# Kernel optimization log

Hardware: AMD Instinct MI355X
Metric: run time of the kernel (lower is better)

Reference implementation:

```python
import jax, jax.numpy as jnp
import numpy as np

B, T, S, H = 4, 256, 1024, 256


def setup_inputs() -> dict:
    key = jax.random.key(0)
    k1, k2, k3, k4, k5, k6 = jax.random.split(key, 6)
    query = jax.random.normal(k1, (B, T, H), dtype=jnp.float32)
    encoder_outputs = jax.random.normal(k2, (B, S, H), dtype=jnp.float32)
    src_lengths = jax.random.randint(k3, (B,), 1, S + 1).astype(jnp.int64)
    scale = 1.0 / np.sqrt(H)
    W_h = jax.random.normal(k4, (H, H), dtype=jnp.float32) * scale
    W_s = jax.random.normal(k5, (H, H), dtype=jnp.float32) * scale
    v = jax.random.normal(k6, (H,), dtype=jnp.float32) * scale
    return {
        "query": query,
        "encoder_outputs": encoder_outputs,
        "src_lengths": src_lengths,
        "W_h": W_h,
        "W_s": W_s,
        "v": v,
    }


def reference(query, encoder_outputs, src_lengths, W_h, W_s, v):
    # score(h_i, s_j) = v^T tanh(W_h h_i + W_s s_j)
    # project once per sequence, then broadcast-add over (tgt, src)
    q_proj = jnp.einsum("bth,hk->btk", query, W_h)            # (B, T, H)
    e_proj = jnp.einsum("bsh,hk->bsk", encoder_outputs, W_s)  # (B, S, H)
    # (B, T, S, H) additive intermediate -> reduce with v
    feats = jnp.tanh(q_proj[:, :, None, :] + e_proj[:, None, :, :])
    scores = jnp.einsum("btsh,h->bts", feats, v)              # (B, T, S)
    # mask padding positions (src positions >= src_lengths[b])
    valid = jnp.arange(scores.shape[-1])[None, :] < src_lengths[:, None]  # (B, S)
    scores = jnp.where(valid[:, None, :], scores, jnp.finfo(scores.dtype).min)
    attn = jax.nn.softmax(scores, axis=-1)                    # (B, T, S)
    attn_out = jnp.einsum("bts,bsh->bth", attn, encoder_outputs)  # (B, T, H)
    return attn_out
```

## Files before the change

### kernel.cpp

```cpp
#include <hip/hip_runtime.h>
#include <math.h>

#define NB 4
#define NT 256
#define NS 1024
#define NH 256
#define TT 4
#define SBK 256
#define NSQ (NS / SBK)
#define BS (NB * NS)

static constexpr float CTWO   = 2.8853900817779268f;
static constexpr float LOG2E  = 1.4426950408889634f;
static constexpr float ACLAMP = 62.0f;

__global__ __launch_bounds__(256) void proj_kernel(const float* __restrict__ Q,
                                                   const float* __restrict__ E,
                                                   const float* __restrict__ W_h,
                                                   const float* __restrict__ W_s,
                                                   float* __restrict__ tq,
                                                   float* __restrict__ te4) {
  __shared__ float As[32][68];
  __shared__ float Bs[32][68];
  const int tid = threadIdx.x;
  int r0 = blockIdx.x * 64;
  const int n0 = blockIdx.y * 64;
  const bool is_q = (r0 < NB * NT);
  const float* A;
  const float* W;
  if (is_q) { A = Q; W = W_h; }
  else      { A = E; W = W_s; r0 -= NB * NT; }
  const int tx = tid & 15;
  const int ty = tid >> 4;
  float acc[4][4] = {};
  for (int k0 = 0; k0 < NH; k0 += 32) {
    {
      const int r = tid >> 2;
      const int kq = (tid & 3) * 8;
      const float* src = A + (size_t)(r0 + r) * NH + k0 + kq;
      float4 v0 = *(const float4*)(src);
      float4 v1 = *(const float4*)(src + 4);
      As[kq + 0][r] = v0.x; As[kq + 1][r] = v0.y; As[kq + 2][r] = v0.z; As[kq + 3][r] = v0.w;
      As[kq + 4][r] = v1.x; As[kq + 5][r] = v1.y; As[kq + 6][r] = v1.z; As[kq + 7][r] = v1.w;
    }
    {
      const int k = tid >> 3;
      const int nq = (tid & 7) * 8;
      const float* src = W + (size_t)(k0 + k) * NH + n0 + nq;
      *(float4*)&Bs[k][nq]     = *(const float4*)(src);
      *(float4*)&Bs[k][nq + 4] = *(const float4*)(src + 4);
    }
    __syncthreads();
    #pragma unroll
    for (int k = 0; k < 32; ++k) {
      float4 a = *(const float4*)&As[k][ty * 4];
      float4 b = *(const float4*)&Bs[k][tx * 4];
      const float av[4] = {a.x, a.y, a.z, a.w};
      const float bv[4] = {b.x, b.y, b.z, b.w};
      #pragma unroll
      for (int i = 0; i < 4; ++i)
        #pragma unroll
        for (int j = 0; j < 4; ++j)
          acc[i][j] = fmaf(av[i], bv[j], acc[i][j]);
    }
    __syncthreads();
  }
  #pragma unroll
  for (int i = 0; i < 4; ++i) {
    float vals[4];
    #pragma unroll
    for (int j = 0; j < 4; ++j) {
      float x = acc[i][j] * CTWO;
      x = fminf(fmaxf(x, -ACLAMP), ACLAMP);
      vals[j] = __builtin_amdgcn_exp2f(x);
    }
    const int r = r0 + ty * 4 + i;
    if (is_q) {
      #pragma unroll
      for (int j = 0; j < 4; ++j)
        tq[(size_t)r * NH + n0 + tx * 4 + j] = vals[j];
    } else {
      const int h4 = (n0 >> 2) + tx;
      float4 w = {vals[0], vals[1], vals[2], vals[3]};
      *(float4*)&te4[((size_t)h4 * BS + r) * 4] = w;
    }
  }
}

__device__ __forceinline__ float allreduce_max(float x, float* red, int tid) {
  #pragma unroll
  for (int o = 32; o > 0; o >>= 1) x = fmaxf(x, __shfl_xor(x, o, 64));
  __syncthreads();
  if ((tid & 63) == 0) red[tid >> 6] = x;
  __syncthreads();
  return fmaxf(fmaxf(red[0], red[1]), fmaxf(red[2], red[3]));
}

__device__ __forceinline__ float allreduce_sum(float x, float* red, int tid) {
  #pragma unroll
  for (int o = 32; o > 0; o >>= 1) x += __shfl_xor(x, o, 64);
  __syncthreads();
  if ((tid & 63) == 0) red[tid >> 6] = x;
  __syncthreads();
  return (red[0] + red[1]) + (red[2] + red[3]);
}

#define PAIR(qa, ea, va, qb, eb, vb, ACC)                                  \
  {                                                                        \
    float ta = fmaf((qa), (ea), 1.0f);                                     \
    float tb = fmaf((qb), (eb), 1.0f);                                     \
    float num = fmaf((va), tb, (vb) * ta);                                 \
    float den = ta * tb;                                                   \
    ACC = fmaf(num, __builtin_amdgcn_rcpf(den), ACC);                      \
  }

__global__ __launch_bounds__(256) void attn_main_kernel(
    const float4* __restrict__ tqq,
    const float4* __restrict__ te4q,
    const float* __restrict__ enc, const int* __restrict__ src_len,
    const float4* __restrict__ vq,
    float* __restrict__ po, float* __restrict__ mbuf, float* __restrict__ lbuf) {
  __shared__ float p_lds[TT][SBK];
  __shared__ float red[4];
  __shared__ float ml[2][TT];
  const int tid = threadIdx.x;
  const int sq = blockIdx.x;
  const int tt = blockIdx.y;
  const int b  = blockIdx.z;
  const int s0 = sq * SBK;
  const int len = src_len[b];
  const int btbase = b * NT + tt * TT;

  if (s0 >= len) {
    #pragma unroll
    for (int t = 0; t < TT; ++t)
      po[((size_t)(btbase + t) * NSQ + sq) * NH + tid] = 0.f;
    if (tid < TT) {
      mbuf[(size_t)(btbase + tid) * NSQ + sq] = -INFINITY;
      lbuf[(size_t)(btbase + tid) * NSQ + sq] = 0.f;
    }
    return;
  }

  float sv = 0.f;
  {
    const float* vf = (const float*)vq;
    sv = vf[tid];
  }
  const float sumv = allreduce_sum(sv, red, tid);

  const int s = s0 + tid;
  const bool valid = s < len;
  const int gs = b * NS + s;

  float acc0[TT], acc1[TT];
  #pragma unroll
  for (int t = 0; t < TT; ++t) { acc0[t] = 0.f; acc1[t] = 0.f; }

  #pragma unroll 8
  for (int h4 = 0; h4 < NH / 4; ++h4) {
    const float4 e = te4q[(size_t)h4 * BS + gs];
    const float4 vv = vq[h4];
    #pragma unroll
    for (int t = 0; t < TT; ++t) {
      const float4 q = tqq[(size_t)(btbase + t) * (NH / 4) + h4];
      PAIR(q.x, e.x, vv.x, q.y, e.y, vv.y, acc0[t]);
      PAIR(q.z, e.z, vv.z, q.w, e.w, vv.w, acc1[t]);
    }
  }

  #pragma unroll
  for (int t = 0; t < TT; ++t) {
    float score = valid ? fmaf(-2.f, acc0[t] + acc1[t], sumv) : -INFINITY;
    float m = allreduce_max(score, red, tid);
    float p = __builtin_amdgcn_exp2f((score - m) * LOG2E);
    float l = allreduce_sum(p, red, tid);
    p_lds[t][tid] = p;
    if (tid == 0) { ml[0][t] = m; ml[1][t] = l; }
  }
  __syncthreads();

  float outv[TT];
  #pragma unroll
  for (int t = 0; t < TT; ++t) outv[t] = 0.f;
  const float* encB = enc + ((size_t)b * NS + s0) * NH + tid;
  for (int sl = 0; sl < SBK; sl += 8) {
    float4 pv[TT][2];
    #pragma unroll
    for (int t = 0; t < TT; ++t) {
      pv[t][0] = *(const float4*)&p_lds[t][sl];
      pv[t][1] = *(const float4*)&p_lds[t][sl + 4];
    }
    float e[8];
    #pragma unroll
    for (int j = 0; j < 8; ++j) e[j] = encB[(size_t)(sl + j) * NH];
    #pragma unroll
    for (int t = 0; t < TT; ++t) {
      outv[t] = fmaf(pv[t][0].x, e[0], outv[t]);
      outv[t] = fmaf(pv[t][0].y, e[1], outv[t]);
      outv[t] = fmaf(pv[t][0].z, e[2], outv[t]);
      outv[t] = fmaf(pv[t][0].w, e[3], outv[t]);
      outv[t] = fmaf(pv[t][1].x, e[4], outv[t]);
      outv[t] = fmaf(pv[t][1].y, e[5], outv[t]);
      outv[t] = fmaf(pv[t][1].z, e[6], outv[t]);
      outv[t] = fmaf(pv[t][1].w, e[7], outv[t]);
    }
  }
  #pragma unroll
  for (int t = 0; t < TT; ++t)
    po[((size_t)(btbase + t) * NSQ + sq) * NH + tid] = outv[t];
  if (tid < TT) {
    mbuf[(size_t)(btbase + tid) * NSQ + sq] = ml[0][tid];
    lbuf[(size_t)(btbase + tid) * NSQ + sq] = ml[1][tid];
  }
}

__global__ __launch_bounds__(256) void combine_kernel(const float* __restrict__ po,
                                                      const float* __restrict__ mbuf,
                                                      const float* __restrict__ lbuf,
                                                      float* __restrict__ out) {
  const int bt = blockIdx.x;
  const int h = threadIdx.x;
  float m[NSQ], l[NSQ];
  float M = -INFINITY;
  #pragma unroll
  for (int i = 0; i < NSQ; ++i) {
    m[i] = mbuf[(size_t)bt * NSQ + i];
    l[i] = lbuf[(size_t)bt * NSQ + i];
    M = fmaxf(M, m[i]);
  }
  float L = 0.f, o = 0.f;
  #pragma unroll
  for (int i = 0; i < NSQ; ++i) {
    float w = __builtin_amdgcn_exp2f((m[i] - M) * LOG2E);
    L = fmaf(w, l[i], L);
    o = fmaf(w, po[((size_t)bt * NSQ + i) * NH + h], o);
  }
  out[(size_t)bt * NH + h] = o / L;
}

extern "C" void kernel_launch(void* const* d_in, const int* in_sizes, int n_in,
                              void* d_out, int out_size, void* d_ws, size_t ws_size,
                              hipStream_t stream) {
  const float* query = (const float*)d_in[0];
  const float* enc   = (const float*)d_in[1];
  const int*   slen  = (const int*)d_in[2];
  const float* W_h   = (const float*)d_in[3];
  const float* W_s   = (const float*)d_in[4];
  const float* v     = (const float*)d_in[5];
  float* out = (float*)d_out;

  float* ws = (float*)d_ws;
  float* tq  = ws;
  float* te4 = tq + (size_t)NB * NT * NH;
  float* po  = te4 + (size_t)NB * NS * NH;
  float* mb  = po + (size_t)NB * NT * NSQ * NH;
  float* lb  = mb + (size_t)NB * NT * NSQ;

  hipLaunchKernelGGL(proj_kernel, dim3((NB * (NT + NS)) / 64, NH / 64), dim3(256), 0, stream,
                     query, enc, W_h, W_s, tq, te4);
  hipLaunchKernelGGL(attn_main_kernel, dim3(NSQ, NT / TT, NB), dim3(256), 0, stream,
                     (const float4*)tq, (const float4*)te4, enc, slen, (const float4*)v,
                     po, mb, lb);
  hipLaunchKernelGGL(combine_kernel, dim3(NB * NT), dim3(256), 0, stream, po, mb, lb, out);
}
```

Before: 75.54 us.

## Restructure attention kernel so each wavefront owns an independent source chunk

The main attention kernel now assigns one 128-source chunk and two target rows to each 64-lane wavefront. Softmax max/sum reductions happen entirely with wave shuffles, which removes the block-wide __syncthreads and shared-memory reductions. Each lane scores two source positions and accumulates the output with float4 encoder loads. Chunks past the source length skip writing zero partial outputs, and the combine kernel skips those chunks. This cuts barrier overhead and changes the tile shape, but doubles the number of partial chunks the combine step reads and uses fewer target rows per pass over the encoder data.

```diff
diff --git a/kernel.cpp b/kernel.cpp
--- a/kernel.cpp
+++ b/kernel.cpp
@@ -5,8 +5,8 @@
 #define NT 256
 #define NS 1024
 #define NH 256
-#define TT 4
-#define SBK 256
+#define TT 2
+#define SBK 128
 #define NSQ (NS / SBK)
 #define BS (NB * NS)
 
@@ -87,24 +87,6 @@
   }
 }
 
-__device__ __forceinline__ float allreduce_max(float x, float* red, int tid) {
-  #pragma unroll
-  for (int o = 32; o > 0; o >>= 1) x = fmaxf(x, __shfl_xor(x, o, 64));
-  __syncthreads();
-  if ((tid & 63) == 0) red[tid >> 6] = x;
-  __syncthreads();
-  return fmaxf(fmaxf(red[0], red[1]), fmaxf(red[2], red[3]));
-}
-
-__device__ __forceinline__ float allreduce_sum(float x, float* red, int tid) {
-  #pragma unroll
-  for (int o = 32; o > 0; o >>= 1) x += __shfl_xor(x, o, 64);
-  __syncthreads();
-  if ((tid & 63) == 0) red[tid >> 6] = x;
-  __syncthreads();
-  return (red[0] + red[1]) + (red[2] + red[3]);
-}
-
 #define PAIR(qa, ea, va, qb, eb, vb, ACC)                                  \
   {                                                                        \
     float ta = fmaf((qa), (ea), 1.0f);                                     \
@@ -117,102 +99,109 @@
 __global__ __launch_bounds__(256) void attn_main_kernel(
     const float4* __restrict__ tqq,
     const float4* __restrict__ te4q,
-    const float* __restrict__ enc, const int* __restrict__ src_len,
+    const float4* __restrict__ enc4,
+    const int* __restrict__ src_len,
     const float4* __restrict__ vq,
-    float* __restrict__ po, float* __restrict__ mbuf, float* __restrict__ lbuf) {
-  __shared__ float p_lds[TT][SBK];
-  __shared__ float red[4];
-  __shared__ float ml[2][TT];
+    float4* __restrict__ po4, float* __restrict__ mbuf, float* __restrict__ lbuf) {
+  __shared__ float p_lds[4][TT][SBK];
   const int tid = threadIdx.x;
-  const int sq = blockIdx.x;
-  const int tt = blockIdx.y;
-  const int b  = blockIdx.z;
+  const int wid = tid >> 6;
+  const int lane = tid & 63;
+  const int bx = blockIdx.x;
+  const int sq = wid * 2 + (bx & 1);
+  const int b  = (bx >> 1) & 3;
+  const int tt = bx >> 3;
+  const int btbase = b * NT + tt * TT;
   const int s0 = sq * SBK;
   const int len = src_len[b];
-  const int btbase = b * NT + tt * TT;
 
   if (s0 >= len) {
-    #pragma unroll
-    for (int t = 0; t < TT; ++t)
-      po[((size_t)(btbase + t) * NSQ + sq) * NH + tid] = 0.f;
-    if (tid < TT) {
-      mbuf[(size_t)(btbase + tid) * NSQ + sq] = -INFINITY;
-      lbuf[(size_t)(btbase + tid) * NSQ + sq] = 0.f;
+    if (lane < TT) {
+      mbuf[(size_t)(btbase + lane) * NSQ + sq] = -INFINITY;
+      lbuf[(size_t)(btbase + lane) * NSQ + sq] = 0.f;
     }
     return;
   }
 
-  float sv = 0.f;
+  float sumv;
   {
-    const float* vf = (const float*)vq;
-    sv = vf[tid];
-  }
-  const float sumv = allreduce_sum(sv, red, tid);
-
-  const int s = s0 + tid;
-  const bool valid = s < len;
-  const int gs = b * NS + s;
-
-  float acc0[TT], acc1[TT];
-  #pragma unroll
-  for (int t = 0; t < TT; ++t) { acc0[t] = 0.f; acc1[t] = 0.f; }
-
-  #pragma unroll 8
+    float4 v4 = vq[lane];
+    float sv = (v4.x + v4.y) + (v4.z + v4.w);
+    #pragma unroll
+    for (int o = 32; o > 0; o >>= 1) sv += __shfl_xor(sv, o, 64);
+    sumv = sv;
+  }
+
+  const int gs0 = b * NS + s0;
+  const int sa = s0 + lane;
+  const int sb = s0 + 64 + lane;
+  const bool va_ok = sa < len;
+  const bool vb_ok = sb < len;
+
+  float accA0[TT], accA1[TT], accB0[TT], accB1[TT];
+  #pragma unroll
+  for (int t = 0; t < TT; ++t) { accA0[t] = accA1[t] = accB0[t] = accB1[t] = 0.f; }
+
+  #pragma unroll 4
   for (int h4 = 0; h4 < NH / 4; ++h4) {
-    const float4 e = te4q[(size_t)h4 * BS + gs];
+    const float4 ea = te4q[(size_t)h4 * BS + gs0 + lane];
+    const float4 eb = te4q[(size_t)h4 * BS + gs0 + 64 + lane];
     const float4 vv = vq[h4];
     #pragma unroll
     for (int t = 0; t < TT; ++t) {
       const float4 q = tqq[(size_t)(btbase + t) * (NH / 4) + h4];
-      PAIR(q.x, e.x, vv.x, q.y, e.y, vv.y, acc0[t]);
-      PAIR(q.z, e.z, vv.z, q.w, e.w, vv.w, acc1[t]);
+      PAIR(q.x, ea.x, vv.x, q.y, ea.y, vv.y, accA0[t]);
+      PAIR(q.z, ea.z, vv.z, q.w, ea.w, vv.w, accA1[t]);
+      PAIR(q.x, eb.x, vv.x, q.y, eb.y, vv.y, accB0[t]);
+      PAIR(q.z, eb.z, vv.z, q.w, eb.w, vv.w, accB1[t]);
     }
   }
 
   #pragma unroll
   for (int t = 0; t < TT; ++t) {
-    float score = valid ? fmaf(-2.f, acc0[t] + acc1[t], sumv) : -INFINITY;
-    float m = allreduce_max(score, red, tid);
-    float p = __builtin_amdgcn_exp2f((score - m) * LOG2E);
-    float l = allreduce_sum(p, red, tid);
-    p_lds[t][tid] = p;
-    if (tid == 0) { ml[0][t] = m; ml[1][t] = l; }
-  }
-  __syncthreads();
-
-  float outv[TT];
-  #pragma unroll
-  for (int t = 0; t < TT; ++t) outv[t] = 0.f;
-  const float* encB = enc + ((size_t)b * NS + s0) * NH + tid;
-  for (int sl = 0; sl < SBK; sl += 8) {
-    float4 pv[TT][2];
+    float xa = va_ok ? fmaf(-2.f, accA0[t] + accA1[t], sumv) : -INFINITY;
+    float xb = vb_ok ? fmaf(-2.f, accB0[t] + accB1[t], sumv) : -INFINITY;
+    float m = fmaxf(xa, xb);
+    #pragma unroll
+    for (int o = 32; o > 0; o >>= 1) m = fmaxf(m, __shfl_xor(m, o, 64));
+    float pa = __builtin_amdgcn_exp2f((xa - m) * LOG2E);
+    float pb = __builtin_amdgcn_exp2f((xb - m) * LOG2E);
+    float l = pa + pb;
+    #pragma unroll
+    for (int o = 32; o > 0; o >>= 1) l += __shfl_xor(l, o, 64);
+    p_lds[wid][t][lane] = pa;
+    p_lds[wid][t][64 + lane] = pb;
+    if (lane == 0) {
+      mbuf[(size_t)(btbase + t) * NSQ + sq] = m;
+      lbuf[(size_t)(btbase + t) * NSQ + sq] = l;
+    }
+  }
+
+  float4 o[TT];
+  #pragma unroll
+  for (int t = 0; t < TT; ++t) o[t] = make_float4(0.f, 0.f, 0.f, 0.f);
+  #pragma unroll 2
+  for (int s = 0; s < SBK; s += 4) {
+    float4 e0 = enc4[(size_t)(gs0 + s + 0) * (NH / 4) + lane];
+    float4 e1 = enc4[(size_t)(gs0 + s + 1) * (NH / 4) + lane];
+    float4 e2 = enc4[(size_t)(gs0 + s + 2) * (NH / 4) + lane];
+    float4 e3 = enc4[(size_t)(gs0 + s + 3) * (NH / 4) + lane];
     #pragma unroll
     for (int t = 0; t < TT; ++t) {
-      pv[t][0] = *(const float4*)&p_lds[t][sl];
-      pv[t][1] = *(const float4*)&p_lds[t][sl + 4];
-    }
-    float e[8];
-    #pragma unroll
-    for (int j = 0; j < 8; ++j) e[j] = encB[(size_t)(sl + j) * NH];
-    #pragma unroll
-    for (int t = 0; t < TT; ++t) {
-      outv[t] = fmaf(pv[t][0].x, e[0], outv[t]);
-      outv[t] = fmaf(pv[t][0].y, e[1], outv[t]);
-      outv[t] = fmaf(pv[t][0].z, e[2], outv[t]);
-      outv[t] = fmaf(pv[t][0].w, e[3], outv[t]);
-      outv[t] = fmaf(pv[t][1].x, e[4], outv[t]);
-      outv[t] = fmaf(pv[t][1].y, e[5], outv[t]);
-      outv[t] = fmaf(pv[t][1].z, e[6], outv[t]);
-      outv[t] = fmaf(pv[t][1].w, e[7], outv[t]);
+      float4 p = *(const float4*)&p_lds[wid][t][s];
+      o[t].x = fmaf(p.x, e0.x, o[t].x); o[t].y = fmaf(p.x, e0.y, o[t].y);
+      o[t].z = fmaf(p.x, e0.z, o[t].z); o[t].w = fmaf(p.x, e0.w, o[t].w);
+      o[t].x = fmaf(p.y, e1.x, o[t].x); o[t].y = fmaf(p.y, e1.y, o[t].y);
+      o[t].z = fmaf(p.y, e1.z, o[t].z); o[t].w = fmaf(p.y, e1.w, o[t].w);
+      o[t].x = fmaf(p.z, e2.x, o[t].x); o[t].y = fmaf(p.z, e2.y, o[t].y);
+      o[t].z = fmaf(p.z, e2.z, o[t].z); o[t].w = fmaf(p.z, e2.w, o[t].w);
+      o[t].x = fmaf(p.w, e3.x, o[t].x); o[t].y = fmaf(p.w, e3.y, o[t].y);
+      o[t].z = fmaf(p.w, e3.z, o[t].z); o[t].w = fmaf(p.w, e3.w, o[t].w);
     }
   }
   #pragma unroll
   for (int t = 0; t < TT; ++t)
-    po[((size_t)(btbase + t) * NSQ + sq) * NH + tid] = outv[t];
-  if (tid < TT) {
-    mbuf[(size_t)(btbase + tid) * NSQ + sq] = ml[0][tid];
-    lbuf[(size_t)(btbase + tid) * NSQ + sq] = ml[1][tid];
-  }
+    po4[((size_t)(btbase + t) * NSQ + sq) * (NH / 4) + lane] = o[t];
 }
 
 __global__ __launch_bounds__(256) void combine_kernel(const float* __restrict__ po,
@@ -232,9 +221,11 @@
   float L = 0.f, o = 0.f;
   #pragma unroll
   for (int i = 0; i < NSQ; ++i) {
-    float w = __builtin_amdgcn_exp2f((m[i] - M) * LOG2E);
-    L = fmaf(w, l[i], L);
-    o = fmaf(w, po[((size_t)bt * NSQ + i) * NH + h], o);
+    if (m[i] > -INFINITY) {
+      float w = __builtin_amdgcn_exp2f((m[i] - M) * LOG2E);
+      L = fmaf(w, l[i], L);
+      o = fmaf(w, po[((size_t)bt * NSQ + i) * NH + h], o);
+    }
   }
   out[(size_t)bt * NH + h] = o / L;
 }
@@ -259,8 +250,8 @@
 
   hipLaunchKernelGGL(proj_kernel, dim3((NB * (NT + NS)) / 64, NH / 64), dim3(256), 0, stream,
                      query, enc, W_h, W_s, tq, te4);
-  hipLaunchKernelGGL(attn_main_kernel, dim3(NSQ, NT / TT, NB), dim3(256), 0, stream,
-                     (const float4*)tq, (const float4*)te4, enc, slen, (const float4*)v,
-                     po, mb, lb);
+  hipLaunchKernelGGL(attn_main_kernel, dim3(NB * (NT / TT) * NSQ / 4), dim3(256), 0, stream,
+                     (const float4*)tq, (const float4*)te4, (const float4*)enc, slen,
+                     (const float4*)v, (float4*)po, mb, lb);
   hipLaunchKernelGGL(combine_kernel, dim3(NB * NT), dim3(256), 0, stream, po, mb, lb, out);
 }
```

Result: faster. 73.88 us (-2.2%).
